# Kernel tuning notes

Measured on AMD Instinct MI355X. Metric: run time of the kernel, lower is better.

## Reference

```python
import jax, jax.numpy as jnp
import numpy as np
from jax import lax

B, N, C = 8, 16384, 96
ROPE_BASE = 10000.0


def _rope(x):
    """Faithful port of the module's RoPE. x: (b, h, w, c).
    Note: the original computes angles over the h axis but, due to torch
    broadcasting of (h, k_max) against (b, h, w, k_max), the rotation is
    applied along the w axis (valid since h == w)."""
    b, h, w, c = x.shape
    k_max = c // 2
    theta = 1.0 / (ROPE_BASE ** (jnp.arange(k_max, dtype=x.dtype) / k_max))  # (k_max,)
    angles = jnp.arange(h, dtype=x.dtype)[:, None] * theta                  # (h, k_max)
    cos = jnp.cos(angles)[None, None, :, :]  # broadcast over w axis
    sin = jnp.sin(angles)[None, None, :, :]
    xr = x.reshape(b, h, w, k_max, 2)
    xre, xim = xr[..., 0], xr[..., 1]
    ore = xre * cos - xim * sin
    oim = xre * sin + xim * cos
    return jnp.stack([ore, oim], axis=-1).reshape(b, h, w, c)


def setup_inputs() -> dict:
    key = jax.random.key(0)
    ks = jax.random.split(key, 5)
    return {
        "x": jax.random.normal(ks[0], (B, N, C), dtype=jnp.float32),
        "qk_w": jax.random.normal(ks[1], (2 * C, C), dtype=jnp.float32) * 0.05,
        "qk_b": jax.random.normal(ks[2], (2 * C,), dtype=jnp.float32) * 0.02,
        "lepe_w": jax.random.normal(ks[3], (C, 1, 3, 3), dtype=jnp.float32) * 0.1,
        "lepe_b": jax.random.normal(ks[4], (C,), dtype=jnp.float32) * 0.02,
        "num_heads": 4,
    }


def reference(x, qk_w, qk_b, lepe_w, lepe_b, num_heads):
    b, n, c = x.shape
    h = w = int(round(n ** 0.5))
    d = c // num_heads
    inv_sqrt_n = float(n) ** (-0.5)

    qk = x @ qk_w.T + qk_b                        # (b, n, 2c)
    q = jax.nn.elu(qk[..., :c]) + 1.0             # (b, n, c)
    k = jax.nn.elu(qk[..., c:]) + 1.0
    v = x

    q_rope = _rope(q.reshape(b, h, w, c)).reshape(b, n, num_heads, d).transpose(0, 2, 1, 3)
    k_rope = _rope(k.reshape(b, h, w, c)).reshape(b, n, num_heads, d).transpose(0, 2, 1, 3)
    qh = q.reshape(b, n, num_heads, d).transpose(0, 2, 1, 3)  # (b, H, n, d)
    kh = k.reshape(b, n, num_heads, d).transpose(0, 2, 1, 3)
    vh = v.reshape(b, n, num_heads, d).transpose(0, 2, 1, 3)

    k_mean = kh.mean(axis=2, keepdims=True)                         # (b, H, 1, d)
    z = 1.0 / (jnp.einsum('bhnd,bhmd->bhnm', qh, k_mean) + 1e-6)    # (b, H, n, 1)
    kv = jnp.einsum('bhnd,bhne->bhde', k_rope * inv_sqrt_n, vh * inv_sqrt_n)  # (b, H, d, d)
    out = jnp.einsum('bhnd,bhde->bhne', q_rope, kv) * z             # (b, H, n, d)
    out = out.transpose(0, 2, 1, 3).reshape(b, n, c)

    # LePE: depthwise 3x3 conv on v laid out as (b, c, h, w)
    v_img = vh.transpose(0, 2, 1, 3).reshape(b, h, w, c).transpose(0, 3, 1, 2)
    lepe = lax.conv_general_dilated(
        v_img, lepe_w, window_strides=(1, 1), padding='SAME',
        feature_group_count=c, dimension_numbers=('NCHW', 'OIHW', 'NCHW'))
    lepe = lepe + lepe_b[None, :, None, None]
    return out + lepe.transpose(0, 2, 3, 1).reshape(b, n, c)
```

## Files before the change

### kernel.cpp

```cpp
#include <hip/hip_runtime.h>


#define NLINE 16384
#define CCH 96
#define XSP 104
#define KTP 136
#define QSP 98
#define OSP 97
#define THETA_COEF 0.2768273412406135f

typedef __attribute__((ext_vector_type(4))) float f32x4;
typedef __attribute__((ext_vector_type(8))) short bf16x8;

__device__ __forceinline__ unsigned short f2bf(float f) {
  unsigned int u = __float_as_uint(f);
  u += 0x7FFFu + ((u >> 16) & 1u);
  return (unsigned short)(u >> 16);
}
__device__ __forceinline__ float bf2f(unsigned short h) {
  return __uint_as_float(((unsigned int)h) << 16);
}
__device__ __forceinline__ void store_bf4(unsigned short* dst, f32x4 v) {
  unsigned long long pk = (unsigned long long)f2bf(v.x)
    | ((unsigned long long)f2bf(v.y) << 16)
    | ((unsigned long long)f2bf(v.z) << 32)
    | ((unsigned long long)f2bf(v.w) << 48);
  *(unsigned long long*)dst = pk;
}

__global__ void prep_w(const float* __restrict__ qkw, unsigned short* __restrict__ wfrag) {
  int u = blockIdx.x * 256 + threadIdx.x;
  if (u >= 2304) return;
  int lane = u & 63;
  int nt = (u >> 6) % 6;
  int rest = u / 384;
  int kk = rest % 3, half = rest / 3;
  int lr = lane & 15, q4 = lane >> 4;
  int row = half * 96 + nt * 16 + lr;
  int col0 = kk * 32 + q4 * 8;
  const float* src = qkw + row * 96 + col0;
  unsigned short* dst = wfrag + (size_t)u * 8;
#pragma unroll
  for (int j = 0; j < 8; ++j) dst[j] = f2bf(src[j]);
}

__global__ __launch_bounds__(256, 3) void la_k1(
    const float* __restrict__ x, const unsigned short* __restrict__ wfrag,
    const float* __restrict__ qkb, float* __restrict__ kv_g,
    float* __restrict__ ksum_g)
{
  const int tid  = threadIdx.x;
  const int b    = blockIdx.x >> 7;
  const int tile = blockIdx.x & 127;

  __shared__ alignas(16) unsigned short xs[128 * XSP];
  __shared__ alignas(16) unsigned short kqt[96 * KTP];
  __shared__ float theta_s[48];
  __shared__ float ksum_s[96];
  __shared__ float biask[96];

  if (tid < 96) { biask[tid] = qkb[96 + tid]; ksum_s[tid] = 0.0f; }
  if (tid < 48) theta_s[tid] = exp2f(-THETA_COEF * (float)tid);

  const float* xb = x + ((size_t)b * NLINE + (size_t)tile * 128) * CCH;
  for (int i = tid; i < 3072; i += 256) {
    int r = i / 24, c4 = i % 24;
    store_bf4(&xs[r * XSP + c4 * 4], ((const f32x4*)xb)[i]);
  }
  __syncthreads();

  const int wave = tid >> 6;
  const int lane = tid & 63;
  const int lr   = lane & 15;
  const int q4   = lane >> 4;
  const int row0 = wave * 32;

  f32x4 acc[2][6];
#pragma unroll
  for (int mt = 0; mt < 2; ++mt)
#pragma unroll
    for (int nt = 0; nt < 6; ++nt) acc[mt][nt] = (f32x4){0.f, 0.f, 0.f, 0.f};

#pragma unroll
  for (int kk = 0; kk < 3; ++kk) {
    const int koff = kk * 32 + q4 * 8;
    bf16x8 a0 = *(const bf16x8*)&xs[(row0 + lr) * XSP + koff];
    bf16x8 a1 = *(const bf16x8*)&xs[(row0 + 16 + lr) * XSP + koff];
#pragma unroll
    for (int nt = 0; nt < 6; ++nt) {
      bf16x8 bf = *(const bf16x8*)&wfrag[(size_t)(((3 + kk) * 6 + nt) * 64 + lane) * 8];
      acc[0][nt] = __builtin_amdgcn_mfma_f32_16x16x32_bf16(a0, bf, acc[0][nt], 0, 0, 0);
      acc[1][nt] = __builtin_amdgcn_mfma_f32_16x16x32_bf16(a1, bf, acc[1][nt], 0, 0, 0);
    }
  }

#pragma unroll
  for (int nt = 0; nt < 6; ++nt) {
    const int col = nt * 16 + lr;
    const float bias = biask[col];
    float csum = 0.0f;
#pragma unroll
    for (int mt = 0; mt < 2; ++mt)
#pragma unroll
      for (int rg = 0; rg < 4; ++rg) {
        int row = row0 + mt * 16 + q4 * 4 + rg;
        float v = acc[mt][nt][rg] + bias;
        v = (v > 0.0f) ? (v + 1.0f) : __expf(v);
        csum += v;
        kqt[col * KTP + row] = f2bf(v);
      }
    atomicAdd(&ksum_s[col], csum);
  }
  __syncthreads();

  if (tid < 96) atomicAdd(&ksum_g[b * 96 + tid], ksum_s[tid]);

  for (int s = 0; s < 24; ++s) {
    int i = tid + 256 * s;
    int cp = i >> 7, r = i & 127;
    float re = bf2f(kqt[(2 * cp) * KTP + r]);
    float im = bf2f(kqt[(2 * cp + 1) * KTP + r]);
    float sn, cn;
    __sincosf((float)r * theta_s[cp], &sn, &cn);
    kqt[(2 * cp) * KTP + r]     = f2bf(re * cn - im * sn);
    kqt[(2 * cp + 1) * KTP + r] = f2bf(re * sn + im * cn);
  }
  __syncthreads();

  const int h = wave;
  f32x4 kvacc[2][2];
#pragma unroll
  for (int mt = 0; mt < 2; ++mt)
#pragma unroll
    for (int nt = 0; nt < 2; ++nt) kvacc[mt][nt] = (f32x4){0.f, 0.f, 0.f, 0.f};

#pragma unroll
  for (int kk = 0; kk < 4; ++kk) {
    const int rbase = kk * 32 + q4 * 8;
    bf16x8 afr[2], bfr[2];
#pragma unroll
    for (int mt = 0; mt < 2; ++mt) {
      int c = 24 * h + mt * 16 + lr; if (c > 95) c = 95;
      afr[mt] = *(const bf16x8*)&kqt[c * KTP + rbase];
    }
#pragma unroll
    for (int nt = 0; nt < 2; ++nt) {
      int c = 24 * h + nt * 16 + lr; if (c > 95) c = 95;
#pragma unroll
      for (int j = 0; j < 8; ++j) bfr[nt][j] = (short)xs[(rbase + j) * XSP + c];
    }
#pragma unroll
    for (int mt = 0; mt < 2; ++mt)
#pragma unroll
      for (int nt = 0; nt < 2; ++nt)
        kvacc[mt][nt] = __builtin_amdgcn_mfma_f32_16x16x32_bf16(afr[mt], bfr[nt], kvacc[mt][nt], 0, 0, 0);
  }

  const float inv_n = 1.0f / 16384.0f;
  float* kvb = kv_g + ((size_t)b * 4 + h) * 576;
#pragma unroll
  for (int mt = 0; mt < 2; ++mt)
#pragma unroll
    for (int rg = 0; rg < 4; ++rg) {
      int d = mt * 16 + q4 * 4 + rg;
      if (d < 24) {
#pragma unroll
        for (int nt = 0; nt < 2; ++nt) {
          int e = nt * 16 + lr;
          if (e < 24) atomicAdd(&kvb[d * 24 + e], kvacc[mt][nt][rg] * inv_n);
        }
      }
    }
}

__global__ __launch_bounds__(256, 3) void la_k2(
    const float* __restrict__ x, const unsigned short* __restrict__ wfrag,
    const float* __restrict__ qkb, const float* __restrict__ lepe_w,
    const float* __restrict__ lepe_b, const float* __restrict__ kv_g,
    const float* __restrict__ ksum_g, float* __restrict__ out)
{
  const int tid = threadIdx.x;
  const int b   = blockIdx.x & 7;
  const int seg = blockIdx.x >> 3;
  const int y   = seg >> 1;

  __shared__ alignas(16) unsigned short xs[64 * XSP];
  __shared__ alignas(16) unsigned short qs[64 * QSP];
  __shared__ float outs[64 * OSP];
  __shared__ float lepe_s[9 * 96];
  __shared__ float theta_s[48];

  if (tid < 48) theta_s[tid] = exp2f(-THETA_COEF * (float)tid);
  for (int i = tid; i < 864; i += 256) {
    int ch = i / 9, tap = i % 9;
    lepe_s[tap * 96 + ch] = lepe_w[i];
  }

  const float* xb = x + ((size_t)b * NLINE + (size_t)seg * 64) * CCH;
  for (int i = tid; i < 1536; i += 256) {
    int t = i / 24, c4 = i % 24;
    store_bf4(&xs[t * XSP + c4 * 4], ((const f32x4*)xb)[i]);
  }
  __syncthreads();

  const int wave = tid >> 6;
  const int lane = tid & 63;
  const int lr   = lane & 15;
  const int q4   = lane >> 4;

  f32x4 acc[6];
#pragma unroll
  for (int nt = 0; nt < 6; ++nt) acc[nt] = (f32x4){0.f, 0.f, 0.f, 0.f};
#pragma unroll
  for (int kk = 0; kk < 3; ++kk) {
    const int koff = kk * 32 + q4 * 8;
    bf16x8 a = *(const bf16x8*)&xs[(wave * 16 + lr) * XSP + koff];
#pragma unroll
    for (int nt = 0; nt < 6; ++nt) {
      bf16x8 bf = *(const bf16x8*)&wfrag[(size_t)((kk * 6 + nt) * 64 + lane) * 8];
      acc[nt] = __builtin_amdgcn_mfma_f32_16x16x32_bf16(a, bf, acc[nt], 0, 0, 0);
    }
  }
#pragma unroll
  for (int nt = 0; nt < 6; ++nt) {
    const int col = nt * 16 + lr;
    const float bias = qkb[col];
#pragma unroll
    for (int rg = 0; rg < 4; ++rg) {
      int t = wave * 16 + q4 * 4 + rg;
      float v = acc[nt][rg] + bias;
      v = (v > 0.0f) ? (v + 1.0f) : __expf(v);
      qs[t * QSP + col] = f2bf(v);
    }
  }
  __syncthreads();

  {
    const int t  = lane;
    const int h  = __builtin_amdgcn_readfirstlane(wave);
    const int xw = ((seg & 1) << 6) + t;
    const float inv_n = 1.0f / 16384.0f;

    float qv[24];
    const unsigned int* qrow = (const unsigned int*)&qs[t * QSP + 24 * h];
#pragma unroll
    for (int u = 0; u < 12; ++u) {
      unsigned int w = qrow[u];
      qv[2 * u]     = bf2f((unsigned short)(w & 0xFFFFu));
      qv[2 * u + 1] = bf2f((unsigned short)(w >> 16));
    }

    const float* km = ksum_g + b * 96 + 24 * h;
    float dot = 0.0f;
#pragma unroll
    for (int d2 = 0; d2 < 24; ++d2) dot += qv[d2] * km[d2];
    const float z = 1.0f / (dot * inv_n + 1e-6f);

    float qr[24];
#pragma unroll
    for (int jj = 0; jj < 12; ++jj) {
      float sn, cn;
      __sincosf((float)xw * theta_s[12 * h + jj], &sn, &cn);
      float re = qv[2 * jj], im = qv[2 * jj + 1];
      qr[2 * jj]     = re * cn - im * sn;
      qr[2 * jj + 1] = re * sn + im * cn;
    }

    const float* kvh = kv_g + ((size_t)b * 4 + h) * 576;
    float res[24];
#pragma unroll
    for (int e = 0; e < 24; ++e) res[e] = 0.0f;
    for (int d2 = 0; d2 < 24; ++d2) {
      float qd = qr[d2];
#pragma unroll
      for (int e = 0; e < 24; ++e) res[e] += qd * kvh[d2 * 24 + e];
    }
    const float* lb = lepe_b + 24 * h;
#pragma unroll
    for (int e = 0; e < 24; ++e) outs[t * OSP + 24 * h + e] = res[e] * z + lb[e];
  }
  __syncthreads();

  float* ob = out + ((size_t)b * NLINE + (size_t)seg * 64) * CCH;
  const float* xg = x + (size_t)b * NLINE * CCH;
#pragma unroll
  for (int k = 0; k < 6; ++k) {
    int idx = tid + 256 * k;
    int tl = idx / 24, c4 = idx % 24;
    int ch0 = c4 * 4;
    int xw = ((seg & 1) << 6) + tl;

    float r0 = outs[tl * OSP + ch0];
    float r1 = outs[tl * OSP + ch0 + 1];
    float r2 = outs[tl * OSP + ch0 + 2];
    float r3 = outs[tl * OSP + ch0 + 3];

#pragma unroll
    for (int dy = 0; dy < 3; ++dy) {
      int yy = y + dy - 1;
      if (yy < 0 || yy > 127) continue;
      const float* rowp = xg + ((size_t)yy * 128) * CCH;
#pragma unroll
      for (int dx = 0; dx < 3; ++dx) {
        int xx = xw + dx - 1;
        if (xx < 0 || xx > 127) continue;
        f32x4 v = *(const f32x4*)(rowp + xx * CCH + ch0);
        const int tap = dy * 3 + dx;
        const float* wp = &lepe_s[tap * 96 + ch0];
        r0 += wp[0] * v.x;
        r1 += wp[1] * v.y;
        r2 += wp[2] * v.z;
        r3 += wp[3] * v.w;
      }
    }
    f32x4 o = { r0, r1, r2, r3 };
    ((f32x4*)ob)[idx] = o;
  }
}

extern "C" void kernel_launch(void* const* d_in, const int* in_sizes, int n_in,
                              void* d_out, int out_size, void* d_ws, size_t ws_size,
                              hipStream_t stream) {
  const float* x      = (const float*)d_in[0];
  const float* qkw    = (const float*)d_in[1];
  const float* qkb    = (const float*)d_in[2];
  const float* lepe_w = (const float*)d_in[3];
  const float* lepe_b = (const float*)d_in[4];
  float* out = (float*)d_out;

  unsigned short* wfrag = (unsigned short*)d_ws;
  float* kv_g   = (float*)((char*)d_ws + 36864);
  float* ksum_g = kv_g + 18432;

  hipMemsetAsync(kv_g, 0, 19200 * sizeof(float), stream);
  prep_w<<<dim3(9), dim3(256), 0, stream>>>(qkw, wfrag);
  la_k1<<<dim3(1024), dim3(256), 0, stream>>>(x, wfrag, qkb, kv_g, ksum_g);
  la_k2<<<dim3(2048), dim3(256), 0, stream>>>(x, wfrag, qkb, lepe_w, lepe_b, kv_g, ksum_g, out);
}
```

Measured before the change: 200.2 us.

## Swizzle LDS tiles, load k2 MFMA fragments from global, shrink k2 smem

In la_k1, the x tile's LDS layout is XOR-swizzled to cut bank conflicts, the bias moves into registers, and RoPE theta is computed incrementally instead of read from a shared table. In la_k2, the shared x tile is dropped so A fragments are loaded straight from global and converted to bf16. The output staging buffer becomes fp16, which shrinks LDS use, and launch bounds rise from 3 to 5 blocks per SU to raise occupancy. Storing the attention output in fp16 adds rounding error, and the tighter launch bound may force register spills.

```diff
diff --git a/kernel.cpp b/kernel.cpp
--- a/kernel.cpp
+++ b/kernel.cpp
@@ -6,7 +6,7 @@
 #define XSP 104
 #define KTP 136
 #define QSP 98
-#define OSP 97
+#define OP2 100
 #define THETA_COEF 0.2768273412406135f
 
 typedef __attribute__((ext_vector_type(4))) float f32x4;
@@ -36,9 +36,7 @@
   int rest = u / 384;
   int kk = rest % 3, half = rest / 3;
   int lr = lane & 15, q4 = lane >> 4;
-  int row = half * 96 + nt * 16 + lr;
-  int col0 = kk * 32 + q4 * 8;
-  const float* src = qkw + row * 96 + col0;
+  const float* src = qkw + (half * 96 + nt * 16 + lr) * 96 + kk * 32 + q4 * 8;
   unsigned short* dst = wfrag + (size_t)u * 8;
 #pragma unroll
   for (int j = 0; j < 8; ++j) dst[j] = f2bf(src[j]);
@@ -55,19 +53,9 @@
 
   __shared__ alignas(16) unsigned short xs[128 * XSP];
   __shared__ alignas(16) unsigned short kqt[96 * KTP];
-  __shared__ float theta_s[48];
   __shared__ float ksum_s[96];
-  __shared__ float biask[96];
-
-  if (tid < 96) { biask[tid] = qkb[96 + tid]; ksum_s[tid] = 0.0f; }
-  if (tid < 48) theta_s[tid] = exp2f(-THETA_COEF * (float)tid);
-
-  const float* xb = x + ((size_t)b * NLINE + (size_t)tile * 128) * CCH;
-  for (int i = tid; i < 3072; i += 256) {
-    int r = i / 24, c4 = i % 24;
-    store_bf4(&xs[r * XSP + c4 * 4], ((const f32x4*)xb)[i]);
-  }
-  __syncthreads();
+
+  if (tid < 96) ksum_s[tid] = 0.0f;
 
   const int wave = tid >> 6;
   const int lane = tid & 63;
@@ -75,6 +63,19 @@
   const int q4   = lane >> 4;
   const int row0 = wave * 32;
 
+  float biasv[6];
+#pragma unroll
+  for (int nt = 0; nt < 6; ++nt) biasv[nt] = qkb[96 + nt * 16 + lr];
+
+  const float* xb = x + ((size_t)b * NLINE + (size_t)tile * 128) * CCH;
+  for (int i = tid; i < 3072; i += 256) {
+    int r = i / 24, c4 = i % 24;
+    int sw = (r >> 3) & 3;
+    store_bf4(&xs[r * XSP + ((((c4 >> 1) ^ sw) << 3) | ((c4 & 1) << 2))],
+              ((const f32x4*)xb)[i]);
+  }
+  __syncthreads();
+
   f32x4 acc[2][6];
 #pragma unroll
   for (int mt = 0; mt < 2; ++mt)
@@ -83,9 +84,10 @@
 
 #pragma unroll
   for (int kk = 0; kk < 3; ++kk) {
-    const int koff = kk * 32 + q4 * 8;
-    bf16x8 a0 = *(const bf16x8*)&xs[(row0 + lr) * XSP + koff];
-    bf16x8 a1 = *(const bf16x8*)&xs[(row0 + 16 + lr) * XSP + koff];
+    const int g = kk * 4 + q4;
+    const int r1 = row0 + lr, r2 = row0 + 16 + lr;
+    bf16x8 a0 = *(const bf16x8*)&xs[r1 * XSP + ((g ^ ((r1 >> 3) & 3)) << 3)];
+    bf16x8 a1 = *(const bf16x8*)&xs[r2 * XSP + ((g ^ ((r2 >> 3) & 3)) << 3)];
 #pragma unroll
     for (int nt = 0; nt < 6; ++nt) {
       bf16x8 bf = *(const bf16x8*)&wfrag[(size_t)(((3 + kk) * 6 + nt) * 64 + lane) * 8];
@@ -97,7 +99,7 @@
 #pragma unroll
   for (int nt = 0; nt < 6; ++nt) {
     const int col = nt * 16 + lr;
-    const float bias = biask[col];
+    const float bias = biasv[nt];
     float csum = 0.0f;
 #pragma unroll
     for (int mt = 0; mt < 2; ++mt)
@@ -115,15 +117,22 @@
 
   if (tid < 96) atomicAdd(&ksum_g[b * 96 + tid], ksum_s[tid]);
 
-  for (int s = 0; s < 24; ++s) {
-    int i = tid + 256 * s;
-    int cp = i >> 7, r = i & 127;
-    float re = bf2f(kqt[(2 * cp) * KTP + r]);
-    float im = bf2f(kqt[(2 * cp + 1) * KTP + r]);
-    float sn, cn;
-    __sincosf((float)r * theta_s[cp], &sn, &cn);
-    kqt[(2 * cp) * KTP + r]     = f2bf(re * cn - im * sn);
-    kqt[(2 * cp + 1) * KTP + r] = f2bf(re * sn + im * cn);
+  {
+    const int r = tid & 127;
+    const int cp0 = tid >> 7;
+    float theta = exp2f(-THETA_COEF * (float)cp0);
+    const float fstep = exp2f(-2.0f * THETA_COEF);
+#pragma unroll 4
+    for (int s = 0; s < 24; ++s) {
+      int cp = cp0 + 2 * s;
+      float re = bf2f(kqt[(2 * cp) * KTP + r]);
+      float im = bf2f(kqt[(2 * cp + 1) * KTP + r]);
+      float sn, cn;
+      __sincosf((float)r * theta, &sn, &cn);
+      kqt[(2 * cp) * KTP + r]     = f2bf(re * cn - im * sn);
+      kqt[(2 * cp + 1) * KTP + r] = f2bf(re * sn + im * cn);
+      theta *= fstep;
+    }
   }
   __syncthreads();
 
@@ -137,6 +146,7 @@
 #pragma unroll
   for (int kk = 0; kk < 4; ++kk) {
     const int rbase = kk * 32 + q4 * 8;
+    const int sw = (rbase >> 3) & 3;
     bf16x8 afr[2], bfr[2];
 #pragma unroll
     for (int mt = 0; mt < 2; ++mt) {
@@ -146,8 +156,9 @@
 #pragma unroll
     for (int nt = 0; nt < 2; ++nt) {
       int c = 24 * h + nt * 16 + lr; if (c > 95) c = 95;
-#pragma unroll
-      for (int j = 0; j < 8; ++j) bfr[nt][j] = (short)xs[(rbase + j) * XSP + c];
+      const int off = (((c >> 3) ^ sw) << 3) | (c & 7);
+#pragma unroll
+      for (int j = 0; j < 8; ++j) bfr[nt][j] = (short)xs[(rbase + j) * XSP + off];
     }
 #pragma unroll
     for (int mt = 0; mt < 2; ++mt)
@@ -173,7 +184,7 @@
     }
 }
 
-__global__ __launch_bounds__(256, 3) void la_k2(
+__global__ __launch_bounds__(256, 5) void la_k2(
     const float* __restrict__ x, const unsigned short* __restrict__ wfrag,
     const float* __restrict__ qkb, const float* __restrict__ lepe_w,
     const float* __restrict__ lepe_b, const float* __restrict__ kv_g,
@@ -184,9 +195,8 @@
   const int seg = blockIdx.x >> 3;
   const int y   = seg >> 1;
 
-  __shared__ alignas(16) unsigned short xs[64 * XSP];
   __shared__ alignas(16) unsigned short qs[64 * QSP];
-  __shared__ float outs[64 * OSP];
+  __shared__ _Float16 outs[64 * OP2];
   __shared__ float lepe_s[9 * 96];
   __shared__ float theta_s[48];
 
@@ -196,35 +206,43 @@
     lepe_s[tap * 96 + ch] = lepe_w[i];
   }
 
-  const float* xb = x + ((size_t)b * NLINE + (size_t)seg * 64) * CCH;
-  for (int i = tid; i < 1536; i += 256) {
-    int t = i / 24, c4 = i % 24;
-    store_bf4(&xs[t * XSP + c4 * 4], ((const f32x4*)xb)[i]);
-  }
-  __syncthreads();
-
   const int wave = tid >> 6;
   const int lane = tid & 63;
   const int lr   = lane & 15;
   const int q4   = lane >> 4;
 
+  float biasv[6];
+#pragma unroll
+  for (int nt = 0; nt < 6; ++nt) biasv[nt] = qkb[nt * 16 + lr];
+
+  const float* xb = x + ((size_t)b * NLINE + (size_t)seg * 64) * CCH;
+  bf16x8 afrag[3];
+#pragma unroll
+  for (int kk = 0; kk < 3; ++kk) {
+    const float* ap = xb + (wave * 16 + lr) * CCH + kk * 32 + q4 * 8;
+    f32x4 v0 = ((const f32x4*)ap)[0];
+    f32x4 v1 = ((const f32x4*)ap)[1];
+    afrag[kk][0] = (short)f2bf(v0.x); afrag[kk][1] = (short)f2bf(v0.y);
+    afrag[kk][2] = (short)f2bf(v0.z); afrag[kk][3] = (short)f2bf(v0.w);
+    afrag[kk][4] = (short)f2bf(v1.x); afrag[kk][5] = (short)f2bf(v1.y);
+    afrag[kk][6] = (short)f2bf(v1.z); afrag[kk][7] = (short)f2bf(v1.w);
+  }
+
   f32x4 acc[6];
 #pragma unroll
   for (int nt = 0; nt < 6; ++nt) acc[nt] = (f32x4){0.f, 0.f, 0.f, 0.f};
 #pragma unroll
   for (int kk = 0; kk < 3; ++kk) {
-    const int koff = kk * 32 + q4 * 8;
-    bf16x8 a = *(const bf16x8*)&xs[(wave * 16 + lr) * XSP + koff];
 #pragma unroll
     for (int nt = 0; nt < 6; ++nt) {
       bf16x8 bf = *(const bf16x8*)&wfrag[(size_t)((kk * 6 + nt) * 64 + lane) * 8];
-      acc[nt] = __builtin_amdgcn_mfma_f32_16x16x32_bf16(a, bf, acc[nt], 0, 0, 0);
+      acc[nt] = __builtin_amdgcn_mfma_f32_16x16x32_bf16(afrag[kk], bf, acc[nt], 0, 0, 0);
     }
   }
 #pragma unroll
   for (int nt = 0; nt < 6; ++nt) {
     const int col = nt * 16 + lr;
-    const float bias = qkb[col];
+    const float bias = biasv[nt];
 #pragma unroll
     for (int rg = 0; rg < 4; ++rg) {
       int t = wave * 16 + q4 * 4 + rg;
@@ -277,7 +295,8 @@
     }
     const float* lb = lepe_b + 24 * h;
 #pragma unroll
-    for (int e = 0; e < 24; ++e) outs[t * OSP + 24 * h + e] = res[e] * z + lb[e];
+    for (int e = 0; e < 24; ++e)
+      outs[t * OP2 + 24 * h + e] = (_Float16)(res[e] * z + lb[e]);
   }
   __syncthreads();
 
@@ -290,10 +309,10 @@
     int ch0 = c4 * 4;
     int xw = ((seg & 1) << 6) + tl;
 
-    float r0 = outs[tl * OSP + ch0];
-    float r1 = outs[tl * OSP + ch0 + 1];
-    float r2 = outs[tl * OSP + ch0 + 2];
-    float r3 = outs[tl * OSP + ch0 + 3];
+    float r0 = (float)outs[tl * OP2 + ch0];
+    float r1 = (float)outs[tl * OP2 + ch0 + 1];
+    float r2 = (float)outs[tl * OP2 + ch0 + 2];
+    float r3 = (float)outs[tl * OP2 + ch0 + 3];
 
 #pragma unroll
     for (int dy = 0; dy < 3; ++dy) {
@@ -305,8 +324,7 @@
         int xx = xw + dx - 1;
         if (xx < 0 || xx > 127) continue;
         f32x4 v = *(const f32x4*)(rowp + xx * CCH + ch0);
-        const int tap = dy * 3 + dx;
-        const float* wp = &lepe_s[tap * 96 + ch0];
+        const float* wp = &lepe_s[(dy * 3 + dx) * 96 + ch0];
         r0 += wp[0] * v.x;
         r1 += wp[1] * v.y;
         r2 += wp[2] * v.z;
```

Result: faster. 184.0 us (-8.1%).
